# Performance work log

Hardware: AMD Instinct MI355X
Metric: run time of the kernel (lower is better)

The kernel has to match this reference:

```python
import jax, jax.numpy as jnp
import numpy as np

K = 3  # from init kwarg


def setup_inputs() -> dict:
    key = jax.random.key(0)
    k1, k2 = jax.random.split(key)
    B, N, D = 32, 2048, 128
    features = jax.random.normal(k1, (B, N, D), dtype=jnp.float32)
    strength = jax.random.uniform(k2, (), dtype=jnp.float32)
    return {"features": features, "strength": strength}


def reference(features, strength):
    B, N, D = features.shape
    k = min(K, N - 1)
    x = jax.lax.stop_gradient(features)  # torch uses features.detach() for the mix path

    # pairwise euclidean distance (torch.cdist, p=2): ||a||^2 + ||b||^2 - 2 a.b
    sq = jnp.sum(x * x, axis=-1)                     # (B, N)
    d2 = sq[:, :, None] + sq[:, None, :] - 2.0 * jnp.einsum('bnd,bmd->bnm', x, x)
    dist = jnp.sqrt(jnp.maximum(d2, 0.0))            # (B, N, N)

    # mask self-distance with +1e6 on the diagonal
    eye = jnp.eye(N, dtype=dist.dtype)
    dist = dist + eye[None, :, :] * 1000000.0

    # k smallest -> top_k of negated distances
    _, idx = jax.lax.top_k(-dist, k)                 # idx: (B, N, k)

    # gather neighbor features: gathered[b,n,j] = x[b, idx[b,n,j]]
    gathered = x[jnp.arange(B)[:, None, None], idx]  # (B, N, k, D)
    mix = jnp.mean(gathered, axis=2)                 # (B, N, D)

    s = jnp.clip(strength, 0.0, 1.0)
    return (1.0 - s) * features + s * mix
```

## Files before the change

kernel.cpp:

```cpp
#include <hip/hip_runtime.h>
#include <cfloat>

#define BB 32
#define NN 2048
#define DD 128
#define RM 128
#define CN 64

typedef __attribute__((ext_vector_type(8))) short short8;
typedef __attribute__((ext_vector_type(4))) float float4v;

__device__ __forceinline__ unsigned short f2bf(float f) {
    unsigned int u = __builtin_bit_cast(unsigned int, f);
    u += 0x7FFFu + ((u >> 16) & 1u);
    return (unsigned short)(u >> 16);
}

__device__ __forceinline__ unsigned int umn(unsigned int a, unsigned int b) { return a < b ? a : b; }
__device__ __forceinline__ unsigned int umx(unsigned int a, unsigned int b) { return a > b ? a : b; }
#define CSU(a, b) { unsigned int _lo = umn(a, b), _hi = umx(a, b); (a) = _lo; (b) = _hi; }

__device__ __forceinline__ void gl2lds16(const unsigned short* g, unsigned short* l) {
    __builtin_amdgcn_global_load_lds(
        (const __attribute__((address_space(1))) void*)g,
        (__attribute__((address_space(3))) void*)l, 16, 0, 0);
}

__global__ __launch_bounds__(256) void prep_kernel(const float* __restrict__ x,
        unsigned short* __restrict__ xb16, float* __restrict__ sq) {
    int t = blockIdx.x * 256 + threadIdx.x;
    int row = t >> 2;
    int q = t & 3;
    const float4* xp = reinterpret_cast<const float4*>(x + (size_t)row * DD + q * 32);
    unsigned short* op = xb16 + (size_t)row * DD + q * 32;
    float acc = 0.f;
#pragma unroll
    for (int i = 0; i < 4; ++i) {
        float4 v0 = xp[2 * i], v1 = xp[2 * i + 1];
        acc += v0.x * v0.x + v0.y * v0.y + v0.z * v0.z + v0.w * v0.w;
        acc += v1.x * v1.x + v1.y * v1.y + v1.z * v1.z + v1.w * v1.w;
        short8 pk;
        pk[0] = (short)f2bf(v0.x); pk[1] = (short)f2bf(v0.y);
        pk[2] = (short)f2bf(v0.z); pk[3] = (short)f2bf(v0.w);
        pk[4] = (short)f2bf(v1.x); pk[5] = (short)f2bf(v1.y);
        pk[6] = (short)f2bf(v1.z); pk[7] = (short)f2bf(v1.w);
        *reinterpret_cast<short8*>(op + i * 8) = pk;
    }
    acc += __shfl_xor(acc, 1);
    acc += __shfl_xor(acc, 2);
    if (q == 0) sq[row] = acc;
}

__global__ __launch_bounds__(256) void sq_kernel(const float* __restrict__ x,
                                                 float* __restrict__ sq) {
    int t = blockIdx.x * 256 + threadIdx.x;
    int row = t >> 2;
    int q = t & 3;
    const float4* xp = reinterpret_cast<const float4*>(x + (size_t)row * DD + q * 32);
    float acc = 0.f;
#pragma unroll
    for (int i = 0; i < 8; ++i) {
        float4 v = xp[i];
        acc += v.x * v.x + v.y * v.y + v.z * v.z + v.w * v.w;
    }
    acc += __shfl_xor(acc, 1);
    acc += __shfl_xor(acc, 2);
    if (q == 0) sq[row] = acc;
}

template<bool PRE>
__global__ __launch_bounds__(256, 2) void knn_kernel(const float* __restrict__ x,
        const unsigned short* __restrict__ xb16g,
        const float* __restrict__ sqv, const float* __restrict__ strength,
        float* __restrict__ out) {
    __shared__ __align__(16) unsigned short btile[2 * CN * DD];
    __shared__ unsigned int cand8[RM * 8];

    const int b = blockIdx.x;
    const int row0 = blockIdx.y * RM;
    const int tid = threadIdx.x;
    const int w = tid >> 6;
    const int lane = tid & 63;
    const int m = lane & 15;
    const int quad = lane >> 4;
    const float* __restrict__ xb = x + (size_t)b * NN * DD;
    const unsigned short* __restrict__ gb = PRE ? xb16g + (size_t)b * NN * DD : nullptr;

    short8 afrag[2][4];
    if constexpr (PRE) {
#pragma unroll
        for (int rg = 0; rg < 2; ++rg)
#pragma unroll
            for (int kc = 0; kc < 4; ++kc)
                afrag[rg][kc] = *reinterpret_cast<const short8*>(
                    gb + (size_t)(row0 + 32 * w + rg * 16 + m) * DD + kc * 32 + quad * 8);
    } else {
#pragma unroll
        for (int rg = 0; rg < 2; ++rg)
#pragma unroll
            for (int kc = 0; kc < 4; ++kc) {
                const float4* src = reinterpret_cast<const float4*>(
                    xb + (size_t)(row0 + 32 * w + rg * 16 + m) * DD + kc * 32 + quad * 8);
                float4 v0 = src[0], v1 = src[1];
                short8 pk;
                pk[0] = (short)f2bf(v0.x); pk[1] = (short)f2bf(v0.y);
                pk[2] = (short)f2bf(v0.z); pk[3] = (short)f2bf(v0.w);
                pk[4] = (short)f2bf(v1.x); pk[5] = (short)f2bf(v1.y);
                pk[6] = (short)f2bf(v1.z); pk[7] = (short)f2bf(v1.w);
                afrag[rg][kc] = pk;
            }
    }

    {
        unsigned short* buf = btile;
        if constexpr (PRE) {
#pragma unroll
            for (int l = 0; l < 4; ++l) {
                int f = (l * 4 + w) * 64 + lane;
                int r = f >> 4, p = f & 15;
                int c = p ^ (r & 7);
                gl2lds16(gb + (size_t)r * DD + c * 8, buf + (l * 4 + w) * 512);
            }
        } else {
#pragma unroll
            for (int l = 0; l < 4; ++l) {
                int id = l * 256 + tid;
                int r = id >> 4, c = id & 15, p = c ^ (r & 7);
                const float4* src = reinterpret_cast<const float4*>(xb + (size_t)r * DD + c * 8);
                float4 v0 = src[0], v1 = src[1];
                short8 pk;
                pk[0] = (short)f2bf(v0.x); pk[1] = (short)f2bf(v0.y);
                pk[2] = (short)f2bf(v0.z); pk[3] = (short)f2bf(v0.w);
                pk[4] = (short)f2bf(v1.x); pk[5] = (short)f2bf(v1.y);
                pk[6] = (short)f2bf(v1.z); pk[7] = (short)f2bf(v1.w);
                *reinterpret_cast<short8*>(buf + r * DD + p * 8) = pk;
            }
        }
    }
    __syncthreads();

    unsigned int tk[2][4][4];
#pragma unroll
    for (int rg = 0; rg < 2; ++rg)
#pragma unroll
        for (int i = 0; i < 4; ++i)
#pragma unroll
            for (int q = 0; q < 4; ++q) tk[rg][i][q] = 0xFFFFFFFFu;

    for (int ct = 0; ct < NN / CN; ++ct) {
        unsigned short* cur = btile + (size_t)(ct & 1) * CN * DD;
        unsigned short* nxt = btile + (size_t)((ct + 1) & 1) * CN * DD;

        if (ct + 1 < NN / CN) {
            int cb = (ct + 1) * CN;
            if constexpr (PRE) {
#pragma unroll
                for (int l = 0; l < 4; ++l) {
                    int f = (l * 4 + w) * 64 + lane;
                    int r = f >> 4, p = f & 15;
                    int c = p ^ (r & 7);
                    gl2lds16(gb + (size_t)(cb + r) * DD + c * 8, nxt + (l * 4 + w) * 512);
                }
            } else {
#pragma unroll
                for (int l = 0; l < 4; ++l) {
                    int id = l * 256 + tid;
                    int r = id >> 4, c = id & 15, p = c ^ (r & 7);
                    const float4* src = reinterpret_cast<const float4*>(xb + (size_t)(cb + r) * DD + c * 8);
                    float4 v0 = src[0], v1 = src[1];
                    short8 pk;
                    pk[0] = (short)f2bf(v0.x); pk[1] = (short)f2bf(v0.y);
                    pk[2] = (short)f2bf(v0.z); pk[3] = (short)f2bf(v0.w);
                    pk[4] = (short)f2bf(v1.x); pk[5] = (short)f2bf(v1.y);
                    pk[6] = (short)f2bf(v1.z); pk[7] = (short)f2bf(v1.w);
                    *reinterpret_cast<short8*>(nxt + r * DD + p * 8) = pk;
                }
            }
        }

        float sqb[4];
#pragma unroll
        for (int cc = 0; cc < 4; ++cc)
            sqb[cc] = sqv[(size_t)b * NN + ct * CN + cc * 16 + m] + 1024.0f;

        float4v acc[2][4];
#pragma unroll
        for (int rg = 0; rg < 2; ++rg)
#pragma unroll
            for (int cc = 0; cc < 4; ++cc) acc[rg][cc] = (float4v){0.f, 0.f, 0.f, 0.f};
#pragma unroll
        for (int kc = 0; kc < 4; ++kc) {
            short8 bfrag[4];
#pragma unroll
            for (int cc = 0; cc < 4; ++cc) {
                int rl = cc * 16 + m;
                int p = (kc * 4 + quad) ^ (m & 7);
                bfrag[cc] = *reinterpret_cast<const short8*>(cur + rl * DD + p * 8);
            }
#pragma unroll
            for (int rg = 0; rg < 2; ++rg)
#pragma unroll
                for (int cc = 0; cc < 4; ++cc)
                    acc[rg][cc] = __builtin_amdgcn_mfma_f32_16x16x32_bf16(
                        afrag[rg][kc], bfrag[cc], acc[rg][cc], 0, 0, 0);
        }

#pragma unroll
        for (int cc = 0; cc < 4; ++cc) {
            unsigned int col = (unsigned int)(ct * CN + cc * 16 + m);
#pragma unroll
            for (int rg = 0; rg < 2; ++rg)
#pragma unroll
                for (int reg = 0; reg < 4; ++reg) {
                    float scb = fmaf(-2.f, acc[rg][cc][reg], sqb[cc]);
                    unsigned int key = (__builtin_bit_cast(unsigned int, scb) & 0xFFFFF800u) | col;
                    unsigned int n;
                    n = umn(tk[rg][reg][0], key); key = umx(tk[rg][reg][0], key); tk[rg][reg][0] = n;
                    n = umn(tk[rg][reg][1], key); key = umx(tk[rg][reg][1], key); tk[rg][reg][1] = n;
                    n = umn(tk[rg][reg][2], key); key = umx(tk[rg][reg][2], key); tk[rg][reg][2] = n;
                    tk[rg][reg][3] = umn(tk[rg][reg][3], key);
                }
        }

        __syncthreads();
    }

#pragma unroll
    for (int rg = 0; rg < 2; ++rg)
#pragma unroll
        for (int reg = 0; reg < 4; ++reg) {
            unsigned int e[8];
#pragma unroll
            for (int j = 0; j < 4; ++j) e[j] = tk[rg][reg][j];
#pragma unroll
            for (int j = 4; j < 8; ++j) e[j] = 0xFFFFFFFFu;
#pragma unroll
            for (int st = 0; st < 4; ++st) {
                int mask = 1 << st;
                unsigned int rv[8];
#pragma unroll
                for (int j = 0; j < 8; ++j)
                    rv[j] = (unsigned int)__shfl_xor((int)e[7 - j], mask, 64);
#pragma unroll
                for (int j = 0; j < 8; ++j) e[j] = umn(e[j], rv[j]);
                CSU(e[0], e[4]); CSU(e[1], e[5]); CSU(e[2], e[6]); CSU(e[3], e[7]);
                CSU(e[0], e[2]); CSU(e[1], e[3]); CSU(e[4], e[6]); CSU(e[5], e[7]);
                CSU(e[0], e[1]); CSU(e[2], e[3]); CSU(e[4], e[5]); CSU(e[6], e[7]);
            }
            if (m == 0) {
                int row = 32 * w + rg * 16 + quad * 4 + reg;
#pragma unroll
                for (int j = 0; j < 8; ++j) cand8[row * 8 + j] = e[j];
            }
        }
    __syncthreads();

    double* refd = reinterpret_cast<double*>(btile);
    int* best3 = reinterpret_cast<int*>(btile) + 2048;

    {
        int r = tid >> 1, h = tid & 1;
        int grow = row0 + r;
        int ci[4];
#pragma unroll
        for (int j = 0; j < 4; ++j) ci[j] = (int)(cand8[r * 8 + h * 4 + j] & 0x7FFu);
        const float* pr = xb + (size_t)grow * DD;
        const float* pc[4];
#pragma unroll
        for (int j = 0; j < 4; ++j) pc[j] = xb + (size_t)ci[j] * DD;
        double a[4] = {0.0, 0.0, 0.0, 0.0};
#pragma unroll 4
        for (int d4 = 0; d4 < 32; ++d4) {
            float4 wv = *reinterpret_cast<const float4*>(pr + d4 * 4);
#pragma unroll
            for (int j = 0; j < 4; ++j) {
                float4 v = *reinterpret_cast<const float4*>(pc[j] + d4 * 4);
                double d;
                d = (double)wv.x - (double)v.x; a[j] += d * d;
                d = (double)wv.y - (double)v.y; a[j] += d * d;
                d = (double)wv.z - (double)v.z; a[j] += d * d;
                d = (double)wv.w - (double)v.w; a[j] += d * d;
            }
        }
#pragma unroll
        for (int j = 0; j < 4; ++j)
            refd[r * 8 + h * 4 + j] = (ci[j] == grow) ? DBL_MAX : a[j];
    }
    __syncthreads();

    if (tid < RM) {
        int r = tid;
        double b0 = DBL_MAX, b1 = DBL_MAX, b2 = DBL_MAX;
        int i0 = 0x7fffffff, i1 = 0x7fffffff, i2 = 0x7fffffff;
        for (int e = 0; e < 8; ++e) {
            double dv = refd[r * 8 + e];
            int ix = (int)(cand8[r * 8 + e] & 0x7FFu);
            if (dv < b2 || (dv == b2 && ix < i2)) {
                b2 = dv; i2 = ix;
                if (b1 > b2 || (b1 == b2 && i1 > i2)) { double td = b1; b1 = b2; b2 = td; int tn = i1; i1 = i2; i2 = tn; }
                if (b0 > b1 || (b0 == b1 && i0 > i1)) { double td = b0; b0 = b1; b1 = td; int tn = i0; i0 = i1; i1 = tn; }
            }
        }
        best3[r * 3 + 0] = i0; best3[r * 3 + 1] = i1; best3[r * 3 + 2] = i2;
    }
    __syncthreads();

    {
        int r = tid >> 1, q = tid & 1;
        float s = fminf(fmaxf(strength[0], 0.f), 1.f);
        const float* pa = xb + (size_t)(row0 + r) * DD + q * 64;
        const float* p1 = xb + (size_t)best3[r * 3 + 0] * DD + q * 64;
        const float* p2 = xb + (size_t)best3[r * 3 + 1] * DD + q * 64;
        const float* p3 = xb + (size_t)best3[r * 3 + 2] * DD + q * 64;
        float* po = out + ((size_t)b * NN + row0 + r) * DD + q * 64;
#pragma unroll
        for (int l = 0; l < 16; ++l) {
            float4 a  = *reinterpret_cast<const float4*>(pa + l * 4);
            float4 n1 = *reinterpret_cast<const float4*>(p1 + l * 4);
            float4 n2 = *reinterpret_cast<const float4*>(p2 + l * 4);
            float4 n3 = *reinterpret_cast<const float4*>(p3 + l * 4);
            float4 o;
            o.x = (1.f - s) * a.x + s * ((n1.x + n2.x + n3.x) / 3.f);
            o.y = (1.f - s) * a.y + s * ((n1.y + n2.y + n3.y) / 3.f);
            o.z = (1.f - s) * a.z + s * ((n1.z + n2.z + n3.z) / 3.f);
            o.w = (1.f - s) * a.w + s * ((n1.w + n2.w + n3.w) / 3.f);
            *reinterpret_cast<float4*>(po + l * 4) = o;
        }
    }
}

extern "C" void kernel_launch(void* const* d_in, const int* in_sizes, int n_in,
                              void* d_out, int out_size, void* d_ws, size_t ws_size,
                              hipStream_t stream) {
    const float* x = (const float*)d_in[0];
    const float* strength = (const float*)d_in[1];
    float* out = (float*)d_out;
    float* sq = (float*)d_ws;
    unsigned short* xb16 = (unsigned short*)((char*)d_ws + 256 * 1024);
    const size_t need = 256 * 1024 + (size_t)BB * NN * DD * sizeof(unsigned short);

    if (ws_size >= need) {
        prep_kernel<<<dim3((BB * NN * 4) / 256), 256, 0, stream>>>(x, xb16, sq);
        knn_kernel<true><<<dim3(BB, NN / RM), 256, 0, stream>>>(x, xb16, sq, strength, out);
    } else {
        sq_kernel<<<dim3((BB * NN * 4) / 256), 256, 0, stream>>>(x, sq);
        knn_kernel<false><<<dim3(BB, NN / RM), 256, 0, stream>>>(x, nullptr, sq, strength, out);
    }
}
```

Measured before the change: 200.5 us.

## Split candidate columns across two wave groups and use med3 top-4 insertion

Each block now runs 512 threads: the four row-waves are duplicated into two column groups, and each group handles half of a 128-column candidate tile. Both groups keep their own top-8 candidate list, and 16 candidates per row are refined in double precision. The per-key sorted insertion into the running top-4 now uses v_med3_u32 instead of a chain of min/max pairs, which shortens the dependency chain. The aim is more waves in flight and fewer ALU ops in the selection hot loop, at the cost of twice the LDS tile size and twice the refinement work.

```diff
diff --git a/kernel.cpp b/kernel.cpp
--- a/kernel.cpp
+++ b/kernel.cpp
@@ -5,7 +5,8 @@
 #define NN 2048
 #define DD 128
 #define RM 128
-#define CN 64
+#define CN 128
+#define NITER (NN / CN)
 
 typedef __attribute__((ext_vector_type(8))) short short8;
 typedef __attribute__((ext_vector_type(4))) float float4v;
@@ -19,6 +20,12 @@
 __device__ __forceinline__ unsigned int umn(unsigned int a, unsigned int b) { return a < b ? a : b; }
 __device__ __forceinline__ unsigned int umx(unsigned int a, unsigned int b) { return a > b ? a : b; }
 #define CSU(a, b) { unsigned int _lo = umn(a, b), _hi = umx(a, b); (a) = _lo; (b) = _hi; }
+
+__device__ __forceinline__ unsigned int umed3(unsigned int a, unsigned int b, unsigned int c) {
+    unsigned int d;
+    asm("v_med3_u32 %0, %1, %2, %3" : "=v"(d) : "v"(a), "v"(b), "v"(c));
+    return d;
+}
 
 __device__ __forceinline__ void gl2lds16(const unsigned short* g, unsigned short* l) {
     __builtin_amdgcn_global_load_lds(
@@ -69,12 +76,12 @@
 }
 
 template<bool PRE>
-__global__ __launch_bounds__(256, 2) void knn_kernel(const float* __restrict__ x,
+__global__ __launch_bounds__(512, 4) void knn_kernel(const float* __restrict__ x,
         const unsigned short* __restrict__ xb16g,
         const float* __restrict__ sqv, const float* __restrict__ strength,
         float* __restrict__ out) {
     __shared__ __align__(16) unsigned short btile[2 * CN * DD];
-    __shared__ unsigned int cand8[RM * 8];
+    __shared__ unsigned int cand[RM * 16];
 
     const int b = blockIdx.x;
     const int row0 = blockIdx.y * RM;
@@ -83,6 +90,8 @@
     const int lane = tid & 63;
     const int m = lane & 15;
     const int quad = lane >> 4;
+    const int wr = w & 3;
+    const int cg = w >> 2;
     const float* __restrict__ xb = x + (size_t)b * NN * DD;
     const unsigned short* __restrict__ gb = PRE ? xb16g + (size_t)b * NN * DD : nullptr;
 
@@ -93,14 +102,14 @@
 #pragma unroll
             for (int kc = 0; kc < 4; ++kc)
                 afrag[rg][kc] = *reinterpret_cast<const short8*>(
-                    gb + (size_t)(row0 + 32 * w + rg * 16 + m) * DD + kc * 32 + quad * 8);
+                    gb + (size_t)(row0 + wr * 32 + rg * 16 + m) * DD + kc * 32 + quad * 8);
     } else {
 #pragma unroll
         for (int rg = 0; rg < 2; ++rg)
 #pragma unroll
             for (int kc = 0; kc < 4; ++kc) {
                 const float4* src = reinterpret_cast<const float4*>(
-                    xb + (size_t)(row0 + 32 * w + rg * 16 + m) * DD + kc * 32 + quad * 8);
+                    xb + (size_t)(row0 + wr * 32 + rg * 16 + m) * DD + kc * 32 + quad * 8);
                 float4 v0 = src[0], v1 = src[1];
                 short8 pk;
                 pk[0] = (short)f2bf(v0.x); pk[1] = (short)f2bf(v0.y);
@@ -116,15 +125,15 @@
         if constexpr (PRE) {
 #pragma unroll
             for (int l = 0; l < 4; ++l) {
-                int f = (l * 4 + w) * 64 + lane;
+                int f = (l * 8 + w) * 64 + lane;
                 int r = f >> 4, p = f & 15;
                 int c = p ^ (r & 7);
-                gl2lds16(gb + (size_t)r * DD + c * 8, buf + (l * 4 + w) * 512);
+                gl2lds16(gb + (size_t)r * DD + c * 8, buf + (l * 8 + w) * 512);
             }
         } else {
 #pragma unroll
             for (int l = 0; l < 4; ++l) {
-                int id = l * 256 + tid;
+                int id = l * 512 + tid;
                 int r = id >> 4, c = id & 15, p = c ^ (r & 7);
                 const float4* src = reinterpret_cast<const float4*>(xb + (size_t)r * DD + c * 8);
                 float4 v0 = src[0], v1 = src[1];
@@ -147,24 +156,24 @@
 #pragma unroll
             for (int q = 0; q < 4; ++q) tk[rg][i][q] = 0xFFFFFFFFu;
 
-    for (int ct = 0; ct < NN / CN; ++ct) {
+    for (int ct = 0; ct < NITER; ++ct) {
         unsigned short* cur = btile + (size_t)(ct & 1) * CN * DD;
         unsigned short* nxt = btile + (size_t)((ct + 1) & 1) * CN * DD;
 
-        if (ct + 1 < NN / CN) {
+        if (ct + 1 < NITER) {
             int cb = (ct + 1) * CN;
             if constexpr (PRE) {
 #pragma unroll
                 for (int l = 0; l < 4; ++l) {
-                    int f = (l * 4 + w) * 64 + lane;
+                    int f = (l * 8 + w) * 64 + lane;
                     int r = f >> 4, p = f & 15;
                     int c = p ^ (r & 7);
-                    gl2lds16(gb + (size_t)(cb + r) * DD + c * 8, nxt + (l * 4 + w) * 512);
+                    gl2lds16(gb + (size_t)(cb + r) * DD + c * 8, nxt + (l * 8 + w) * 512);
                 }
             } else {
 #pragma unroll
                 for (int l = 0; l < 4; ++l) {
-                    int id = l * 256 + tid;
+                    int id = l * 512 + tid;
                     int r = id >> 4, c = id & 15, p = c ^ (r & 7);
                     const float4* src = reinterpret_cast<const float4*>(xb + (size_t)(cb + r) * DD + c * 8);
                     float4 v0 = src[0], v1 = src[1];
@@ -181,7 +190,7 @@
         float sqb[4];
 #pragma unroll
         for (int cc = 0; cc < 4; ++cc)
-            sqb[cc] = sqv[(size_t)b * NN + ct * CN + cc * 16 + m] + 1024.0f;
+            sqb[cc] = sqv[(size_t)b * NN + ct * CN + cg * 64 + cc * 16 + m] + 1024.0f;
 
         float4v acc[2][4];
 #pragma unroll
@@ -193,7 +202,7 @@
             short8 bfrag[4];
 #pragma unroll
             for (int cc = 0; cc < 4; ++cc) {
-                int rl = cc * 16 + m;
+                int rl = cg * 64 + cc * 16 + m;
                 int p = (kc * 4 + quad) ^ (m & 7);
                 bfrag[cc] = *reinterpret_cast<const short8*>(cur + rl * DD + p * 8);
             }
@@ -207,18 +216,19 @@
 
 #pragma unroll
         for (int cc = 0; cc < 4; ++cc) {
-            unsigned int col = (unsigned int)(ct * CN + cc * 16 + m);
+            unsigned int col = (unsigned int)(ct * CN + cg * 64 + cc * 16 + m);
 #pragma unroll
             for (int rg = 0; rg < 2; ++rg)
 #pragma unroll
                 for (int reg = 0; reg < 4; ++reg) {
                     float scb = fmaf(-2.f, acc[rg][cc][reg], sqb[cc]);
                     unsigned int key = (__builtin_bit_cast(unsigned int, scb) & 0xFFFFF800u) | col;
-                    unsigned int n;
-                    n = umn(tk[rg][reg][0], key); key = umx(tk[rg][reg][0], key); tk[rg][reg][0] = n;
-                    n = umn(tk[rg][reg][1], key); key = umx(tk[rg][reg][1], key); tk[rg][reg][1] = n;
-                    n = umn(tk[rg][reg][2], key); key = umx(tk[rg][reg][2], key); tk[rg][reg][2] = n;
-                    tk[rg][reg][3] = umn(tk[rg][reg][3], key);
+                    unsigned int t0 = tk[rg][reg][0], t1 = tk[rg][reg][1];
+                    unsigned int t2 = tk[rg][reg][2], t3 = tk[rg][reg][3];
+                    tk[rg][reg][0] = umn(t0, key);
+                    tk[rg][reg][1] = umed3(t0, t1, key);
+                    tk[rg][reg][2] = umed3(t1, t2, key);
+                    tk[rg][reg][3] = umed3(t2, t3, key);
                 }
         }
 
@@ -248,22 +258,22 @@
                 CSU(e[0], e[1]); CSU(e[2], e[3]); CSU(e[4], e[5]); CSU(e[6], e[7]);
             }
             if (m == 0) {
-                int row = 32 * w + rg * 16 + quad * 4 + reg;
-#pragma unroll
-                for (int j = 0; j < 8; ++j) cand8[row * 8 + j] = e[j];
+                int row = wr * 32 + rg * 16 + quad * 4 + reg;
+#pragma unroll
+                for (int j = 0; j < 8; ++j) cand[row * 16 + cg * 8 + j] = e[j];
             }
         }
     __syncthreads();
 
     double* refd = reinterpret_cast<double*>(btile);
-    int* best3 = reinterpret_cast<int*>(btile) + 2048;
+    int* best3 = reinterpret_cast<int*>(btile) + 4096;
 
     {
-        int r = tid >> 1, h = tid & 1;
+        int r = tid >> 2, h = tid & 3;
         int grow = row0 + r;
         int ci[4];
 #pragma unroll
-        for (int j = 0; j < 4; ++j) ci[j] = (int)(cand8[r * 8 + h * 4 + j] & 0x7FFu);
+        for (int j = 0; j < 4; ++j) ci[j] = (int)(cand[r * 16 + h * 4 + j] & 0x7FFu);
         const float* pr = xb + (size_t)grow * DD;
         const float* pc[4];
 #pragma unroll
@@ -284,7 +294,7 @@
         }
 #pragma unroll
         for (int j = 0; j < 4; ++j)
-            refd[r * 8 + h * 4 + j] = (ci[j] == grow) ? DBL_MAX : a[j];
+            refd[r * 16 + h * 4 + j] = (ci[j] == grow) ? DBL_MAX : a[j];
     }
     __syncthreads();
 
@@ -292,9 +302,9 @@
         int r = tid;
         double b0 = DBL_MAX, b1 = DBL_MAX, b2 = DBL_MAX;
         int i0 = 0x7fffffff, i1 = 0x7fffffff, i2 = 0x7fffffff;
-        for (int e = 0; e < 8; ++e) {
-            double dv = refd[r * 8 + e];
-            int ix = (int)(cand8[r * 8 + e] & 0x7FFu);
+        for (int e = 0; e < 16; ++e) {
+            double dv = refd[r * 16 + e];
+            int ix = (int)(cand[r * 16 + e] & 0x7FFu);
             if (dv < b2 || (dv == b2 && ix < i2)) {
                 b2 = dv; i2 = ix;
                 if (b1 > b2 || (b1 == b2 && i1 > i2)) { double td = b1; b1 = b2; b2 = td; int tn = i1; i1 = i2; i2 = tn; }
@@ -306,15 +316,15 @@
     __syncthreads();
 
     {
-        int r = tid >> 1, q = tid & 1;
+        int r = tid >> 2, q = tid & 3;
         float s = fminf(fmaxf(strength[0], 0.f), 1.f);
-        const float* pa = xb + (size_t)(row0 + r) * DD + q * 64;
-        const float* p1 = xb + (size_t)best3[r * 3 + 0] * DD + q * 64;
-        const float* p2 = xb + (size_t)best3[r * 3 + 1] * DD + q * 64;
-        const float* p3 = xb + (size_t)best3[r * 3 + 2] * DD + q * 64;
-        float* po = out + ((size_t)b * NN + row0 + r) * DD + q * 64;
-#pragma unroll
-        for (int l = 0; l < 16; ++l) {
+        const float* pa = xb + (size_t)(row0 + r) * DD + q * 32;
+        const float* p1 = xb + (size_t)best3[r * 3 + 0] * DD + q * 32;
+        const float* p2 = xb + (size_t)best3[r * 3 + 1] * DD + q * 32;
+        const float* p3 = xb + (size_t)best3[r * 3 + 2] * DD + q * 32;
+        float* po = out + ((size_t)b * NN + row0 + r) * DD + q * 32;
+#pragma unroll
+        for (int l = 0; l < 8; ++l) {
             float4 a  = *reinterpret_cast<const float4*>(pa + l * 4);
             float4 n1 = *reinterpret_cast<const float4*>(p1 + l * 4);
             float4 n2 = *reinterpret_cast<const float4*>(p2 + l * 4);
@@ -341,9 +351,9 @@
 
     if (ws_size >= need) {
         prep_kernel<<<dim3((BB * NN * 4) / 256), 256, 0, stream>>>(x, xb16, sq);
-        knn_kernel<true><<<dim3(BB, NN / RM), 256, 0, stream>>>(x, xb16, sq, strength, out);
+        knn_kernel<true><<<dim3(BB, NN / RM), 512, 0, stream>>>(x, xb16, sq, strength, out);
     } else {
         sq_kernel<<<dim3((BB * NN * 4) / 256), 256, 0, stream>>>(x, sq);
-        knn_kernel<false><<<dim3(BB, NN / RM), 256, 0, stream>>>(x, nullptr, sq, strength, out);
-    }
-}
+        knn_kernel<false><<<dim3(BB, NN / RM), 512, 0, stream>>>(x, nullptr, sq, strength, out);
+    }
+}
```

Measured after the change: 241.6 us. 1.21x slower.
